# Kernel optimization log

Measured on AMD Instinct MI355X. Metric: run time of the kernel, lower is better.

Reference implementation:

```python
import jax, jax.numpy as jnp
import numpy as np

B, S, D, F, E, K = 2, 2048, 1024, 1024, 8, 2


def setup_inputs() -> dict:
    key = jax.random.key(0)
    kx, kg, k1, k3, k2 = jax.random.split(key, 5)
    # kaiming_uniform_(a=sqrt(5)) => Uniform(-1/sqrt(fan_in), 1/sqrt(fan_in))
    x = jax.random.normal(kx, (B, S, D), dtype=jnp.float32)
    gate_w = jax.random.uniform(kg, (E, D), jnp.float32, -1.0, 1.0) / np.sqrt(D)
    w1 = jax.random.uniform(k1, (E, F, D), jnp.float32, -1.0, 1.0) / np.sqrt(D)
    w3 = jax.random.uniform(k3, (E, F, D), jnp.float32, -1.0, 1.0) / np.sqrt(D)
    w2 = jax.random.uniform(k2, (E, D, F), jnp.float32, -1.0, 1.0) / np.sqrt(F)
    return {"x": x, "gate_w": gate_w, "w1": w1, "w3": w3, "w2": w2}


def reference(x, gate_w, w1, w3, w2):
    b, s, d = x.shape
    T = b * s
    xf = x.reshape(T, d)                      # [T, D]
    # ---- Gate: softmax scores, top-k selection, renormalized weights ----
    logits = xf @ gate_w.T                    # [T, E]
    probs = jax.nn.softmax(logits, axis=-1)
    topk_w, topk_idx = jax.lax.top_k(probs, K)            # [T, K]
    topk_w = topk_w / jnp.sum(topk_w, axis=-1, keepdims=True)
    # Dense per-token gate matrix [T, E]; zero for unselected experts, so the
    # weighted combine below is exactly sum_k w_k * expert_{idx_k}(x).
    gate_full = jnp.zeros((T, E), x.dtype).at[
        jnp.arange(T)[:, None], topk_idx].add(topk_w)
    # ---- Grouped SwiGLU experts: loop over small fixed E, vectorized over tokens ----
    out = jnp.zeros_like(xf)
    for e in range(E):
        h = jax.nn.silu(xf @ w1[e].T) * (xf @ w3[e].T)    # [T, F]
        out = out + gate_full[:, e:e + 1] * (h @ w2[e].T)  # [T, D]
    return out.reshape(b, s, d)
```

## Files before the change

kernel.cpp:

```cpp
#include <hip/hip_runtime.h>
#include <hip/hip_bf16.h>
#include <cstdint>
#include <cstddef>

#define T_TOK 4096
#define DDIM  1024
#define FDIM  1024
#define NEXP  8

typedef __attribute__((ext_vector_type(8))) short bf16x8;
typedef __attribute__((ext_vector_type(4))) float f32x4;
typedef __attribute__((ext_vector_type(8))) unsigned short u16x8;

__device__ __forceinline__ unsigned short f2bf(float f) {
  unsigned int u = __float_as_uint(f);
  u += 0x7FFFu + ((u >> 16) & 1u);
  return (unsigned short)(u >> 16);
}
__device__ __forceinline__ float bf2f(unsigned short u) {
  return __uint_as_float(((unsigned int)u) << 16);
}

__device__ __forceinline__ void gload_lds16(const void* g, void* l) {
  __builtin_amdgcn_global_load_lds(
      (const __attribute__((address_space(1))) unsigned int*)g,
      (__attribute__((address_space(3))) unsigned int*)l, 16, 0, 0);
}

__device__ __forceinline__ void vwait6() { asm volatile("s_waitcnt vmcnt(6)" ::: "memory"); }
__device__ __forceinline__ void vwait4() { asm volatile("s_waitcnt vmcnt(4)" ::: "memory"); }
__device__ __forceinline__ void vwait0() { asm volatile("s_waitcnt vmcnt(0)" ::: "memory"); }
__device__ __forceinline__ void lwait0() { asm volatile("s_waitcnt lgkmcnt(0)" ::: "memory"); }
__device__ __forceinline__ void barr()   { asm volatile("s_barrier" ::: "memory"); }

__device__ __forceinline__ bf16x8 frag_ld(const unsigned short* tile, int row, int kk) {
  int byteoff = (row << 7) + ((kk * 2) ^ ((row & 7) << 4));
  return *reinterpret_cast<const bf16x8*>(reinterpret_cast<const char*>(tile) + byteoff);
}

__device__ __forceinline__ bf16x8 frag_ld32(const unsigned short* tile, int row, int kk) {
  int byteoff = (row << 6) + ((kk * 2) ^ (((row >> 1) & 3) << 4));
  return *reinterpret_cast<const bf16x8*>(reinterpret_cast<const char*>(tile) + byteoff);
}

__global__ __launch_bounds__(256) void prep_kernel(
    const float* __restrict__ w1, const float* __restrict__ w3,
    unsigned short* __restrict__ W1b, unsigned short* __restrict__ W3b,
    const float* __restrict__ x, const float* __restrict__ gw,
    unsigned int* __restrict__ Xb32, int* __restrict__ tkidx, float* __restrict__ tkw,
    int* __restrict__ curp) {
  __shared__ float gws[NEXP * DDIM];
  const int bid = blockIdx.x;
  const int tid = threadIdx.x;

  if (bid < 2048) {
    const int sub = bid >> 10;
    const int b = bid & 1023;
    const float* s = (sub == 0) ? w1 : w3;
    unsigned short* d = (sub == 0) ? W1b : W3b;
    const int n = NEXP * FDIM * DDIM;
    const int stride = 1024 * 256 * 8;
    for (int i = (b * 256 + tid) * 8; i < n; i += stride) {
      float4 a = *reinterpret_cast<const float4*>(s + i);
      float4 c = *reinterpret_cast<const float4*>(s + i + 4);
      u16x8 o;
      o[0] = f2bf(a.x); o[1] = f2bf(a.y); o[2] = f2bf(a.z); o[3] = f2bf(a.w);
      o[4] = f2bf(c.x); o[5] = f2bf(c.y); o[6] = f2bf(c.z); o[7] = f2bf(c.w);
      *reinterpret_cast<u16x8*>(d + i) = o;
    }
    return;
  }

  const int lane = tid & 63;
  const int wid = tid >> 6;
  if (bid == 2048 && tid < NEXP) curp[tid * 32] = 0;
  for (int i = tid; i < NEXP * DDIM / 4; i += 256)
    reinterpret_cast<float4*>(gws)[i] = reinterpret_cast<const float4*>(gw)[i];
  __syncthreads();

  const int t = (bid - 2048) * 4 + wid;
  const float2* xr = reinterpret_cast<const float2*>(x + (size_t)t * DDIM);
  float2 xv[8];
#pragma unroll
  for (int i = 0; i < 8; ++i) xv[i] = xr[i * 64 + lane];
#pragma unroll
  for (int i = 0; i < 8; ++i)
    Xb32[(size_t)t * 512 + i * 64 + lane] =
        (unsigned int)f2bf(xv[i].x) | ((unsigned int)f2bf(xv[i].y) << 16);
  float p[NEXP];
#pragma unroll
  for (int e = 0; e < NEXP; ++e) p[e] = 0.f;
#pragma unroll
  for (int i = 0; i < 8; ++i) {
    const int k = (i * 64 + lane) * 2;
#pragma unroll
    for (int e = 0; e < NEXP; ++e)
      p[e] += xv[i].x * gws[e * DDIM + k] + xv[i].y * gws[e * DDIM + k + 1];
  }
#pragma unroll
  for (int s = 32; s > 0; s >>= 1)
#pragma unroll
    for (int e = 0; e < NEXP; ++e) p[e] += __shfl_xor(p[e], s, 64);
  if (lane == 0) {
    int i0 = 0; float l0 = p[0];
#pragma unroll
    for (int e = 1; e < NEXP; ++e) if (p[e] > l0) { l0 = p[e]; i0 = e; }
    int i1 = -1; float l1 = -1e30f;
#pragma unroll
    for (int e = 0; e < NEXP; ++e) if (e != i0 && p[e] > l1) { l1 = p[e]; i1 = e; }
    float ex = __expf(l1 - l0);
    float w0 = 1.f / (1.f + ex);
    float w1v = ex / (1.f + ex);
    tkidx[t * 2] = i0; tkidx[t * 2 + 1] = i1;
    tkw[t * 2] = w0;   tkw[t * 2 + 1] = w1v;
  }
}

__global__ __launch_bounds__(256) void fill_kernel(const int* __restrict__ tkidx,
                                                   const float* __restrict__ tkw,
                                                   int* __restrict__ offp,
                                                   int* __restrict__ curp,
                                                   int* __restrict__ list,
                                                   float* __restrict__ rgate) {
  __shared__ int ghist[4][NEXP];
  __shared__ int lhist[NEXP], base[NEXP];
  const int tid = threadIdx.x;
  if (tid < 32) ghist[tid >> 3][tid & 7] = 0;
  if (tid < NEXP) lhist[tid] = 0;
  __syncthreads();
  for (int i = tid; i < 2 * T_TOK; i += 256)
    atomicAdd(&ghist[tid >> 6][tkidx[i]], 1);
  const int t = blockIdx.x * 256 + tid;
  const int e0 = tkidx[t * 2], e1 = tkidx[t * 2 + 1];
  const int r0 = atomicAdd(&lhist[e0], 1);
  const int r1 = atomicAdd(&lhist[e1], 1);
  __syncthreads();
  if (tid < NEXP) {
    int o = 0;
#pragma unroll
    for (int j = 0; j < NEXP; ++j) {
      int c = ghist[0][j] + ghist[1][j] + ghist[2][j] + ghist[3][j];
      if (j < tid) o += c;
    }
    if (blockIdx.x == 0) {
      offp[tid] = o;
      if (tid == NEXP - 1)
        offp[NEXP] = o + ghist[0][tid] + ghist[1][tid] + ghist[2][tid] + ghist[3][tid];
    }
    base[tid] = o + atomicAdd(&curp[tid * 32], lhist[tid]);
  }
  __syncthreads();
  const int p0 = base[e0] + r0;
  const int p1 = base[e1] + r1;
  list[p0] = (t << 1);     rgate[p0] = tkw[t * 2];
  list[p1] = (t << 1) | 1; rgate[p1] = tkw[t * 2 + 1];
}

__global__ __launch_bounds__(256) void gemm1_kernel(
    const unsigned short* __restrict__ Xb, const unsigned short* __restrict__ W1b,
    const unsigned short* __restrict__ W3b, unsigned short* __restrict__ Hb,
    const int* __restrict__ off, const int* __restrict__ list,
    const float* __restrict__ w2, unsigned short* __restrict__ W2b) {
  const int bid0 = blockIdx.x;
  const int tid = threadIdx.x;

  if (bid0 < 1024) {
    const int n = NEXP * FDIM * DDIM;
    const int stride = 1024 * 256 * 8;
    for (int i = (bid0 * 256 + tid) * 8; i < n; i += stride) {
      float4 a = *reinterpret_cast<const float4*>(w2 + i);
      float4 c = *reinterpret_cast<const float4*>(w2 + i + 4);
      u16x8 o;
      o[0] = f2bf(a.x); o[1] = f2bf(a.y); o[2] = f2bf(a.z); o[3] = f2bf(a.w);
      o[4] = f2bf(c.x); o[5] = f2bf(c.y); o[6] = f2bf(c.z); o[7] = f2bf(c.w);
      *reinterpret_cast<u16x8*>(W2b + i) = o;
    }
    return;
  }

  const int g = bid0 - 1024;
  const int bx = g & 15;
  const int by = g >> 4;
  const int e = by >> 5;
  const int rt = by & 31;
  const int seg0 = off[e];
  const int Ne = off[e + 1] - seg0;
  const int rowbase = rt * 128;
  if (rowbase >= Ne) return;
  const int f0 = bx * 64;

  __shared__ unsigned short As[2][128 * 32];
  __shared__ unsigned short B1s[2][64 * 32];
  __shared__ unsigned short B3s[2][64 * 32];

  const int lane = tid & 63;
  const int wid = tid >> 6;
  const int wr = wid >> 1, wc = wid & 1;

  int ldsoffA[2]; size_t abase[2];
#pragma unroll
  for (int j = 0; j < 2; ++j) {
    int boff = j * 4096 + wid * 1024 + lane * 16;
    int row = boff >> 6;
    int c = ((boff >> 4) & 3) ^ ((row >> 1) & 3);
    ldsoffA[j] = (j * 4096 + wid * 1024) >> 1;
    int ar = rowbase + row; if (ar > Ne - 1) ar = Ne - 1;
    int tok = list[seg0 + ar] >> 1;
    abase[j] = (size_t)tok * DDIM + c * 8;
  }
  int ldsoffB; size_t bbase;
  {
    int boff = wid * 1024 + lane * 16;
    int row = boff >> 6;
    int c = ((boff >> 4) & 3) ^ ((row >> 1) & 3);
    ldsoffB = (wid * 1024) >> 1;
    bbase = (size_t)(e * FDIM + f0 + row) * DDIM + c * 8;
  }

  f32x4 acc1[4][2], acc3[4][2];
  const f32x4 z = {0.f, 0.f, 0.f, 0.f};
#pragma unroll
  for (int m = 0; m < 4; ++m)
#pragma unroll
    for (int n = 0; n < 2; ++n) { acc1[m][n] = z; acc3[m][n] = z; }

  auto stage = [&](int buf, int kt) {
    const int ko = kt * 32;
#pragma unroll
    for (int j = 0; j < 2; ++j)
      gload_lds16(Xb + abase[j] + ko, &As[buf][ldsoffA[j]]);
    gload_lds16(W1b + bbase + ko, &B1s[buf][ldsoffB]);
    gload_lds16(W3b + bbase + ko, &B3s[buf][ldsoffB]);
  };

  const int lrow = lane & 15;
  const int kb = (lane >> 4) * 8;

  vwait0();
  stage(0, 0);
  stage(1, 1);
  vwait4();
  barr();

  for (int t = 0; t < 32; ++t) {
    const int b = t & 1;
    bf16x8 a[4], p[2], q[2];
#pragma unroll
    for (int m = 0; m < 4; ++m)
      a[m] = frag_ld32(&As[b][0], wr * 64 + m * 16 + lrow, kb);
#pragma unroll
    for (int n = 0; n < 2; ++n) {
      p[n] = frag_ld32(&B1s[b][0], wc * 32 + n * 16 + lrow, kb);
      q[n] = frag_ld32(&B3s[b][0], wc * 32 + n * 16 + lrow, kb);
    }
#pragma unroll
    for (int m = 0; m < 4; ++m)
#pragma unroll
      for (int n = 0; n < 2; ++n) {
        acc1[m][n] = __builtin_amdgcn_mfma_f32_16x16x32_bf16(a[m], p[n], acc1[m][n], 0, 0, 0);
        acc3[m][n] = __builtin_amdgcn_mfma_f32_16x16x32_bf16(a[m], q[n], acc3[m][n], 0, 0, 0);
      }
    if (t == 31) break;
    lwait0();
    barr();
    if (t + 2 < 32) stage(b, t + 2);
    if (t < 30) vwait4(); else vwait0();
    barr();
  }

#pragma unroll
  for (int m = 0; m < 4; ++m)
#pragma unroll
    for (int n = 0; n < 2; ++n)
#pragma unroll
      for (int r = 0; r < 4; ++r) {
        int rloc = wr * 64 + m * 16 + ((lane >> 4) << 2) + r;
        if (rowbase + rloc < Ne) {
          float v1 = acc1[m][n][r], v3 = acc3[m][n][r];
          float h = v1 / (1.f + __expf(-v1)) * v3;
          int col = f0 + wc * 32 + n * 16 + (lane & 15);
          Hb[(size_t)(seg0 + rowbase + rloc) * FDIM + col] = f2bf(h);
        }
      }
}

__global__ __launch_bounds__(256) void gemm2_kernel(
    const unsigned short* __restrict__ Hb, const unsigned short* __restrict__ W2b,
    unsigned short* __restrict__ Yb, const int* __restrict__ off,
    const int* __restrict__ list, const float* __restrict__ rgate) {
  const int e = blockIdx.y >> 5;
  const int rt = blockIdx.y & 31;
  const int seg0 = off[e];
  const int Ne = off[e + 1] - seg0;
  const int rowbase = rt * 128;
  if (rowbase >= Ne) return;
  const int d0 = blockIdx.x * 64;

  __shared__ unsigned short As[2][128 * 64];
  __shared__ unsigned short Bs[2][64 * 64];

  const int tid = threadIdx.x;
  const int lane = tid & 63;
  const int wid = tid >> 6;
  const int wr = wid >> 1, wc = wid & 1;

  int ldsoffA[4]; size_t abase[4];
  int ldsoffB[2]; size_t bbase[2];
#pragma unroll
  for (int j = 0; j < 4; ++j) {
    int boff = j * 4096 + wid * 1024 + lane * 16;
    int row = boff >> 7;
    int c = ((boff >> 4) & 7) ^ (row & 7);
    ldsoffA[j] = (j * 4096 + wid * 1024) >> 1;
    int ar = rowbase + row; if (ar > Ne - 1) ar = Ne - 1;
    abase[j] = (size_t)(seg0 + ar) * FDIM + c * 8;
  }
#pragma unroll
  for (int j = 0; j < 2; ++j) {
    int boff = j * 4096 + wid * 1024 + lane * 16;
    int row = boff >> 7;
    int c = ((boff >> 4) & 7) ^ (row & 7);
    ldsoffB[j] = (j * 4096 + wid * 1024) >> 1;
    bbase[j] = (size_t)(e * DDIM + d0 + row) * FDIM + c * 8;
  }

  f32x4 acc[4][2];
  const f32x4 z = {0.f, 0.f, 0.f, 0.f};
#pragma unroll
  for (int m = 0; m < 4; ++m)
#pragma unroll
    for (int n = 0; n < 2; ++n) acc[m][n] = z;

  auto stage = [&](int buf, int kt) {
    const int ko = kt * 64;
#pragma unroll
    for (int j = 0; j < 4; ++j)
      gload_lds16(Hb + abase[j] + ko, &As[buf][ldsoffA[j]]);
#pragma unroll
    for (int j = 0; j < 2; ++j)
      gload_lds16(W2b + bbase[j] + ko, &Bs[buf][ldsoffB[j]]);
  };

  const int lrow = lane & 15;
  const int kb = (lane >> 4) * 8;

  vwait0();
  stage(0, 0);
  stage(1, 1);
  vwait6();
  barr();

  for (int t = 0; t < 16; ++t) {
    const int b = t & 1;
#pragma unroll
    for (int ks = 0; ks < 2; ++ks) {
      bf16x8 a[4], bb[2];
#pragma unroll
      for (int m = 0; m < 4; ++m)
        a[m] = frag_ld(As[b], wr * 64 + m * 16 + lrow, ks * 32 + kb);
#pragma unroll
      for (int n = 0; n < 2; ++n)
        bb[n] = frag_ld(Bs[b], wc * 32 + n * 16 + lrow, ks * 32 + kb);
#pragma unroll
      for (int m = 0; m < 4; ++m)
#pragma unroll
        for (int n = 0; n < 2; ++n)
          acc[m][n] = __builtin_amdgcn_mfma_f32_16x16x32_bf16(a[m], bb[n], acc[m][n], 0, 0, 0);
    }
    if (t == 15) break;
    lwait0();
    barr();
    if (t + 2 < 16) stage(b, t + 2);
    if (t < 14) vwait6(); else vwait0();
    barr();
  }

#pragma unroll
  for (int m = 0; m < 4; ++m)
#pragma unroll
    for (int r = 0; r < 4; ++r) {
      int rloc = wr * 64 + m * 16 + ((lane >> 4) << 2) + r;
      if (rowbase + rloc < Ne) {
        int rg = seg0 + rowbase + rloc;
        int tk = list[rg];
        float gsc = rgate[rg];
#pragma unroll
        for (int n = 0; n < 2; ++n) {
          int col = d0 + wc * 32 + n * 16 + (lane & 15);
          Yb[(size_t)tk * DDIM + col] = f2bf(gsc * acc[m][n][r]);
        }
      }
    }
}

__global__ __launch_bounds__(256) void combine_kernel(const unsigned short* __restrict__ Yb,
                                                      float* __restrict__ out) {
  const int n = T_TOK * DDIM / 8;
  const int stride = gridDim.x * blockDim.x;
  for (int i = blockIdx.x * blockDim.x + threadIdx.x; i < n; i += stride) {
    int t = i >> 7;
    int c = (i & 127) * 8;
    u16x8 a = *reinterpret_cast<const u16x8*>(Yb + ((size_t)t * 2) * DDIM + c);
    u16x8 b = *reinterpret_cast<const u16x8*>(Yb + ((size_t)t * 2 + 1) * DDIM + c);
    float4 o0, o1;
    o0.x = bf2f(a[0]) + bf2f(b[0]); o0.y = bf2f(a[1]) + bf2f(b[1]);
    o0.z = bf2f(a[2]) + bf2f(b[2]); o0.w = bf2f(a[3]) + bf2f(b[3]);
    o1.x = bf2f(a[4]) + bf2f(b[4]); o1.y = bf2f(a[5]) + bf2f(b[5]);
    o1.z = bf2f(a[6]) + bf2f(b[6]); o1.w = bf2f(a[7]) + bf2f(b[7]);
    float* dst = out + (size_t)t * DDIM + c;
    *reinterpret_cast<float4*>(dst) = o0;
    *reinterpret_cast<float4*>(dst + 4) = o1;
  }
}

extern "C" void kernel_launch(void* const* d_in, const int* in_sizes, int n_in,
                              void* d_out, int out_size, void* d_ws, size_t ws_size,
                              hipStream_t stream) {
  (void)in_sizes; (void)n_in; (void)ws_size; (void)out_size;
  const float* x  = (const float*)d_in[0];
  const float* gw = (const float*)d_in[1];
  const float* w1 = (const float*)d_in[2];
  const float* w3 = (const float*)d_in[3];
  const float* w2 = (const float*)d_in[4];
  float* out = (float*)d_out;

  char* ws = (char*)d_ws;
  unsigned short* Xb  = (unsigned short*)(ws + 0);
  unsigned short* W1b = (unsigned short*)(ws + 8388608);
  unsigned short* W3b = (unsigned short*)(ws + 25165824);
  unsigned short* W2b = (unsigned short*)(ws + 41943040);
  unsigned short* Hb  = (unsigned short*)(ws + 58720256);
  unsigned short* Yb  = (unsigned short*)(ws + 8388608);
  int*   ctrl  = (int*)(ws + 75497472);
  int*   off  = ctrl;
  int*   curp = ctrl + 16;
  int*   tkidx = (int*)(ws + 75497472 + 4096);
  float* tkw   = (float*)(ws + 75497472 + 4096 + 32768);
  int*   list  = (int*)(ws + 75497472 + 4096 + 65536);
  float* rgate = (float*)(ws + 75497472 + 4096 + 98304);

  prep_kernel<<<3072, 256, 0, stream>>>(w1, w3, W1b, W3b,
                                        x, gw, (unsigned int*)Xb, tkidx, tkw, curp);
  fill_kernel<<<16, 256, 0, stream>>>(tkidx, tkw, off, curp, list, rgate);

  gemm1_kernel<<<1024 + 4096, 256, 0, stream>>>(Xb, W1b, W3b, Hb, off, list, w2, W2b);
  gemm2_kernel<<<dim3(16, 256), 256, 0, stream>>>(Hb, W2b, Yb, off, list, rgate);
  combine_kernel<<<2048, 256, 0, stream>>>(Yb, out);
}
```

Before: 160.6 us.

## Compact expert row-tile work map and retile gemm1 to 128x32 with K=64

The fill kernel now builds a compact list of (expert, row-tile) work items, and both GEMMs index blocks through it, so the launch grid no longer contains mostly-empty blocks that exit early. gemm1 switches from 128x64 tiles with K-step 32 to 128x32 tiles with K-step 64, using the 128-byte swizzled layout. This gives each block more MFMAs per barrier and doubles the number of F tiles for parallelism, but each wave now holds fewer accumulators. The W2 conversion blocks are moved to the end of the gemm1 grid, so they are scheduled after the GEMM blocks.

```diff
diff --git a/kernel.cpp b/kernel.cpp
--- a/kernel.cpp
+++ b/kernel.cpp
@@ -28,18 +28,12 @@
 }
 
 __device__ __forceinline__ void vwait6() { asm volatile("s_waitcnt vmcnt(6)" ::: "memory"); }
-__device__ __forceinline__ void vwait4() { asm volatile("s_waitcnt vmcnt(4)" ::: "memory"); }
 __device__ __forceinline__ void vwait0() { asm volatile("s_waitcnt vmcnt(0)" ::: "memory"); }
 __device__ __forceinline__ void lwait0() { asm volatile("s_waitcnt lgkmcnt(0)" ::: "memory"); }
 __device__ __forceinline__ void barr()   { asm volatile("s_barrier" ::: "memory"); }
 
 __device__ __forceinline__ bf16x8 frag_ld(const unsigned short* tile, int row, int kk) {
   int byteoff = (row << 7) + ((kk * 2) ^ ((row & 7) << 4));
-  return *reinterpret_cast<const bf16x8*>(reinterpret_cast<const char*>(tile) + byteoff);
-}
-
-__device__ __forceinline__ bf16x8 frag_ld32(const unsigned short* tile, int row, int kk) {
-  int byteoff = (row << 6) + ((kk * 2) ^ (((row >> 1) & 3) << 4));
   return *reinterpret_cast<const bf16x8*>(reinterpret_cast<const char*>(tile) + byteoff);
 }
 
@@ -121,7 +115,9 @@
                                                    int* __restrict__ offp,
                                                    int* __restrict__ curp,
                                                    int* __restrict__ list,
-                                                   float* __restrict__ rgate) {
+                                                   float* __restrict__ rgate,
+                                                   int* __restrict__ wmap,
+                                                   int* __restrict__ nwp) {
   __shared__ int ghist[4][NEXP];
   __shared__ int lhist[NEXP], base[NEXP];
   const int tid = threadIdx.x;
@@ -135,6 +131,15 @@
   const int r0 = atomicAdd(&lhist[e0], 1);
   const int r1 = atomicAdd(&lhist[e1], 1);
   __syncthreads();
+  if (blockIdx.x == 0 && tid == 64) {
+    int nw = 0;
+    for (int e = 0; e < NEXP; ++e) {
+      int c = ghist[0][e] + ghist[1][e] + ghist[2][e] + ghist[3][e];
+      int nrt = (c + 127) >> 7;
+      for (int r = 0; r < nrt; ++r) wmap[nw++] = (e << 8) | r;
+    }
+    nwp[0] = nw;
+  }
   if (tid < NEXP) {
     int o = 0;
 #pragma unroll
@@ -160,14 +165,16 @@
     const unsigned short* __restrict__ Xb, const unsigned short* __restrict__ W1b,
     const unsigned short* __restrict__ W3b, unsigned short* __restrict__ Hb,
     const int* __restrict__ off, const int* __restrict__ list,
+    const int* __restrict__ wmap, const int* __restrict__ nwp,
     const float* __restrict__ w2, unsigned short* __restrict__ W2b) {
   const int bid0 = blockIdx.x;
   const int tid = threadIdx.x;
 
-  if (bid0 < 1024) {
+  if (bid0 >= 72 * 32) {
+    const int b = bid0 - 72 * 32;
     const int n = NEXP * FDIM * DDIM;
     const int stride = 1024 * 256 * 8;
-    for (int i = (bid0 * 256 + tid) * 8; i < n; i += stride) {
+    for (int i = (b * 256 + tid) * 8; i < n; i += stride) {
       float4 a = *reinterpret_cast<const float4*>(w2 + i);
       float4 c = *reinterpret_cast<const float4*>(w2 + i + 4);
       u16x8 o;
@@ -178,31 +185,31 @@
     return;
   }
 
-  const int g = bid0 - 1024;
-  const int bx = g & 15;
-  const int by = g >> 4;
-  const int e = by >> 5;
-  const int rt = by & 31;
+  const int slot = bid0 >> 5;
+  const int ft = bid0 & 31;
+  if (slot >= nwp[0]) return;
+  const int ent = wmap[slot];
+  const int e = ent >> 8;
+  const int rt = ent & 255;
   const int seg0 = off[e];
   const int Ne = off[e + 1] - seg0;
   const int rowbase = rt * 128;
-  if (rowbase >= Ne) return;
-  const int f0 = bx * 64;
-
-  __shared__ unsigned short As[2][128 * 32];
-  __shared__ unsigned short B1s[2][64 * 32];
-  __shared__ unsigned short B3s[2][64 * 32];
+  const int f0 = ft * 32;
+
+  __shared__ unsigned short As[2][128 * 64];
+  __shared__ unsigned short B1s[2][32 * 64];
+  __shared__ unsigned short B3s[2][32 * 64];
 
   const int lane = tid & 63;
   const int wid = tid >> 6;
   const int wr = wid >> 1, wc = wid & 1;
 
-  int ldsoffA[2]; size_t abase[2];
-#pragma unroll
-  for (int j = 0; j < 2; ++j) {
+  int ldsoffA[4]; size_t abase[4];
+#pragma unroll
+  for (int j = 0; j < 4; ++j) {
     int boff = j * 4096 + wid * 1024 + lane * 16;
-    int row = boff >> 6;
-    int c = ((boff >> 4) & 3) ^ ((row >> 1) & 3);
+    int row = boff >> 7;
+    int c = ((boff >> 4) & 7) ^ (row & 7);
     ldsoffA[j] = (j * 4096 + wid * 1024) >> 1;
     int ar = rowbase + row; if (ar > Ne - 1) ar = Ne - 1;
     int tok = list[seg0 + ar] >> 1;
@@ -210,24 +217,22 @@
   }
   int ldsoffB; size_t bbase;
   {
-    int boff = wid * 1024 + lane * 16;
-    int row = boff >> 6;
-    int c = ((boff >> 4) & 3) ^ ((row >> 1) & 3);
+    int boff = tid * 16;
+    int row = boff >> 7;
+    int c = ((boff >> 4) & 7) ^ (row & 7);
     ldsoffB = (wid * 1024) >> 1;
     bbase = (size_t)(e * FDIM + f0 + row) * DDIM + c * 8;
   }
 
-  f32x4 acc1[4][2], acc3[4][2];
+  f32x4 acc1[4], acc3[4];
   const f32x4 z = {0.f, 0.f, 0.f, 0.f};
 #pragma unroll
-  for (int m = 0; m < 4; ++m)
-#pragma unroll
-    for (int n = 0; n < 2; ++n) { acc1[m][n] = z; acc3[m][n] = z; }
+  for (int m = 0; m < 4; ++m) { acc1[m] = z; acc3[m] = z; }
 
   auto stage = [&](int buf, int kt) {
-    const int ko = kt * 32;
-#pragma unroll
-    for (int j = 0; j < 2; ++j)
+    const int ko = kt * 64;
+#pragma unroll
+    for (int j = 0; j < 4; ++j)
       gload_lds16(Xb + abase[j] + ko, &As[buf][ldsoffA[j]]);
     gload_lds16(W1b + bbase + ko, &B1s[buf][ldsoffB]);
     gload_lds16(W3b + bbase + ko, &B3s[buf][ldsoffB]);
@@ -239,62 +244,63 @@
   vwait0();
   stage(0, 0);
   stage(1, 1);
-  vwait4();
+  vwait6();
   barr();
 
-  for (int t = 0; t < 32; ++t) {
+  for (int t = 0; t < 16; ++t) {
     const int b = t & 1;
-    bf16x8 a[4], p[2], q[2];
-#pragma unroll
-    for (int m = 0; m < 4; ++m)
-      a[m] = frag_ld32(&As[b][0], wr * 64 + m * 16 + lrow, kb);
-#pragma unroll
-    for (int n = 0; n < 2; ++n) {
-      p[n] = frag_ld32(&B1s[b][0], wc * 32 + n * 16 + lrow, kb);
-      q[n] = frag_ld32(&B3s[b][0], wc * 32 + n * 16 + lrow, kb);
-    }
-#pragma unroll
-    for (int m = 0; m < 4; ++m)
-#pragma unroll
-      for (int n = 0; n < 2; ++n) {
-        acc1[m][n] = __builtin_amdgcn_mfma_f32_16x16x32_bf16(a[m], p[n], acc1[m][n], 0, 0, 0);
-        acc3[m][n] = __builtin_amdgcn_mfma_f32_16x16x32_bf16(a[m], q[n], acc3[m][n], 0, 0, 0);
+#pragma unroll
+    for (int ks = 0; ks < 2; ++ks) {
+      bf16x8 a[4], p, q;
+#pragma unroll
+      for (int m = 0; m < 4; ++m)
+        a[m] = frag_ld(As[b], wr * 64 + m * 16 + lrow, ks * 32 + kb);
+      p = frag_ld(B1s[b], wc * 16 + lrow, ks * 32 + kb);
+      q = frag_ld(B3s[b], wc * 16 + lrow, ks * 32 + kb);
+#pragma unroll
+      for (int m = 0; m < 4; ++m) {
+        acc1[m] = __builtin_amdgcn_mfma_f32_16x16x32_bf16(a[m], p, acc1[m], 0, 0, 0);
+        acc3[m] = __builtin_amdgcn_mfma_f32_16x16x32_bf16(a[m], q, acc3[m], 0, 0, 0);
       }
-    if (t == 31) break;
+    }
+    if (t == 15) break;
     lwait0();
     barr();
-    if (t + 2 < 32) stage(b, t + 2);
-    if (t < 30) vwait4(); else vwait0();
+    if (t + 2 < 16) stage(b, t + 2);
+    if (t < 14) vwait6(); else vwait0();
     barr();
   }
 
 #pragma unroll
   for (int m = 0; m < 4; ++m)
 #pragma unroll
-    for (int n = 0; n < 2; ++n)
-#pragma unroll
-      for (int r = 0; r < 4; ++r) {
-        int rloc = wr * 64 + m * 16 + ((lane >> 4) << 2) + r;
-        if (rowbase + rloc < Ne) {
-          float v1 = acc1[m][n][r], v3 = acc3[m][n][r];
-          float h = v1 / (1.f + __expf(-v1)) * v3;
-          int col = f0 + wc * 32 + n * 16 + (lane & 15);
-          Hb[(size_t)(seg0 + rowbase + rloc) * FDIM + col] = f2bf(h);
-        }
+    for (int r = 0; r < 4; ++r) {
+      int rloc = wr * 64 + m * 16 + ((lane >> 4) << 2) + r;
+      if (rowbase + rloc < Ne) {
+        float v1 = acc1[m][r], v3 = acc3[m][r];
+        float h = v1 / (1.f + __expf(-v1)) * v3;
+        int col = f0 + wc * 16 + (lane & 15);
+        Hb[(size_t)(seg0 + rowbase + rloc) * FDIM + col] = f2bf(h);
       }
+    }
 }
 
 __global__ __launch_bounds__(256) void gemm2_kernel(
     const unsigned short* __restrict__ Hb, const unsigned short* __restrict__ W2b,
     unsigned short* __restrict__ Yb, const int* __restrict__ off,
-    const int* __restrict__ list, const float* __restrict__ rgate) {
-  const int e = blockIdx.y >> 5;
-  const int rt = blockIdx.y & 31;
+    const int* __restrict__ list, const float* __restrict__ rgate,
+    const int* __restrict__ wmap, const int* __restrict__ nwp) {
+  const int bid0 = blockIdx.x;
+  const int slot = bid0 >> 4;
+  const int dt = bid0 & 15;
+  if (slot >= nwp[0]) return;
+  const int ent = wmap[slot];
+  const int e = ent >> 8;
+  const int rt = ent & 255;
   const int seg0 = off[e];
   const int Ne = off[e + 1] - seg0;
   const int rowbase = rt * 128;
-  if (rowbase >= Ne) return;
-  const int d0 = blockIdx.x * 64;
+  const int d0 = dt * 64;
 
   __shared__ unsigned short As[2][128 * 64];
   __shared__ unsigned short Bs[2][64 * 64];
@@ -432,8 +438,10 @@
   unsigned short* Hb  = (unsigned short*)(ws + 58720256);
   unsigned short* Yb  = (unsigned short*)(ws + 8388608);
   int*   ctrl  = (int*)(ws + 75497472);
-  int*   off  = ctrl;
-  int*   curp = ctrl + 16;
+  int*   off   = ctrl;
+  int*   nwp   = ctrl + 12;
+  int*   curp  = ctrl + 16;
+  int*   wmap  = ctrl + 256;
   int*   tkidx = (int*)(ws + 75497472 + 4096);
   float* tkw   = (float*)(ws + 75497472 + 4096 + 32768);
   int*   list  = (int*)(ws + 75497472 + 4096 + 65536);
@@ -441,9 +449,10 @@
 
   prep_kernel<<<3072, 256, 0, stream>>>(w1, w3, W1b, W3b,
                                         x, gw, (unsigned int*)Xb, tkidx, tkw, curp);
-  fill_kernel<<<16, 256, 0, stream>>>(tkidx, tkw, off, curp, list, rgate);
-
-  gemm1_kernel<<<1024 + 4096, 256, 0, stream>>>(Xb, W1b, W3b, Hb, off, list, w2, W2b);
-  gemm2_kernel<<<dim3(16, 256), 256, 0, stream>>>(Hb, W2b, Yb, off, list, rgate);
+  fill_kernel<<<16, 256, 0, stream>>>(tkidx, tkw, off, curp, list, rgate, wmap, nwp);
+
+  gemm1_kernel<<<72 * 32 + 1024, 256, 0, stream>>>(Xb, W1b, W3b, Hb, off, list,
+                                                   wmap, nwp, w2, W2b);
+  gemm2_kernel<<<72 * 16, 256, 0, stream>>>(Hb, W2b, Yb, off, list, rgate, wmap, nwp);
   combine_kernel<<<2048, 256, 0, stream>>>(Yb, out);
 }
```

After: 132.9 us. -17.2%, faster.
